# Optimization experiments

Measured on AMD Instinct MI355X. Metric: run time of the kernel, lower is better.

Reference implementation:

```python
import jax, jax.numpy as jnp
import numpy as np

B, N, D = 4096, 128, 256


def setup_inputs() -> dict:
    key = jax.random.key(0)
    ks = jax.random.split(key, 6)
    return {
        "label": jax.random.normal(ks[0], (B, N, D), dtype=jnp.float32),
        "adj_in": jax.random.uniform(ks[1], (N, N), dtype=jnp.float32),
        "adj_out": jax.random.uniform(ks[2], (N, N), dtype=jnp.float32),
        "edge_bias": jnp.zeros((N, D), dtype=jnp.float32),
        "gate_weight": jax.random.normal(ks[3], (D, 1), dtype=jnp.float32) * (6.0 / (D + 1)) ** 0.5,
        "bias_gate": jnp.zeros((N, 1), dtype=jnp.float32),
        "out_edge_bias": jnp.zeros((N, D), dtype=jnp.float32),
        "out_gate_weight": jax.random.normal(ks[4], (D, 1), dtype=jnp.float32) * (6.0 / (D + 1)) ** 0.5,
        "out_bias_gate": jnp.zeros((N, 1), dtype=jnp.float32),
        "loop_gate": jax.random.normal(ks[5], (D, 1), dtype=jnp.float32) * (6.0 / (D + 1)) ** 0.5,
    }


def reference(label, adj_in, adj_out, edge_bias, gate_weight, bias_gate,
              out_edge_bias, out_gate_weight, out_bias_gate, loop_gate):
    h = label  # [B, N, D]
    # origin_adj is a constant buffer in the original module (detached numpy)
    origin = jax.lax.stop_gradient(jnp.where(adj_in <= 0, adj_in, 1.0))

    # in-arc branch: masked dense adjacency matmul + bias + scalar gate
    h_in = jnp.einsum('mn,bnd->bmd', origin * adj_in, h)            # [B, N, D]
    in_gate = jnp.einsum('bnd,do->bno', h, gate_weight) + bias_gate  # [B, N, 1]
    msg_in = (h_in + edge_bias) * jax.nn.sigmoid(in_gate)

    # out-arc branch: transposed mask times out adjacency
    h_out = jnp.einsum('mn,bnd->bmd', origin.T * adj_out, h)
    out_gate = jnp.einsum('bnd,do->bno', h, out_gate_weight) + out_bias_gate
    msg_out = (h_out + out_edge_bias) * jax.nn.sigmoid(out_gate)

    # self-loop branch
    lp_gate = jnp.einsum('bnd,do->bno', h, loop_gate)
    msg_loop = h * jax.nn.sigmoid(lp_gate)

    # dropout p=0.0 -> identity
    return jax.nn.relu(msg_in + msg_out + msg_loop)
```

## Files before the change

kernel.cpp:

```cpp
#include <hip/hip_runtime.h>
#include <hip/hip_bf16.h>

#define NN 128
#define ND 256

typedef __attribute__((ext_vector_type(8))) short short8v;
typedef __attribute__((ext_vector_type(4))) short short4v;
typedef __attribute__((ext_vector_type(4))) float floatx4;

__device__ __forceinline__ unsigned short f2bf(float x){
  unsigned u = __float_as_uint(x);
  u += 0x7FFF + ((u >> 16) & 1);
  return (unsigned short)(u >> 16);
}
__device__ __forceinline__ float bf2f(unsigned short h){
  return __uint_as_float(((unsigned)h) << 16);
}

__global__ void prep_A(const float* __restrict__ adj_in, const float* __restrict__ adj_out,
                       const float* __restrict__ gw, const float* __restrict__ ogw,
                       const float* __restrict__ lw, unsigned short* __restrict__ Abf){
  int idx = blockIdx.x * 256 + threadIdx.x;
  if (idx < 32768){
    int m = idx >> 7, n = idx & 127;
    float v;
    if (m < NN){
      float a = adj_in[m * NN + n];
      v = (a <= 0.f) ? a * a : a;
    } else {
      int mm = m - NN;
      float t = adj_in[n * NN + mm];
      float o = (t <= 0.f) ? t : 1.f;
      v = o * adj_out[mm * NN + n];
    }
    Abf[idx] = f2bf(v);
  } else if (idx < 32768 + 4096){
    int t   = idx - 32768;
    int j   = t & 7, m16 = (t >> 3) & 15, g = (t >> 7) & 3, kc = t >> 9;
    int d   = kc * 32 + 8 * g + j;
    float v = (m16 == 0) ? gw[d] : (m16 == 1) ? ogw[d] : (m16 == 2) ? lw[d] : 0.f;
    Abf[idx] = f2bf(v);
  }
}

__global__ __launch_bounds__(512, 4) void gcn_main(
    const float* __restrict__ H, const unsigned short* __restrict__ Abf,
    const float* __restrict__ eb,  const float* __restrict__ bg,
    const float* __restrict__ oeb, const float* __restrict__ obg,
    float* __restrict__ Out)
{
  __shared__ __align__(16) unsigned short Ht[ND * NN];
  __shared__ float sigS[3 * NN];

  const int tid  = threadIdx.x;
  const int wave = tid >> 6;
  const int lane = tid & 63;
  const int g    = lane >> 4;
  const int m16  = lane & 15;
  const int b    = blockIdx.x;
  const float* Hb = H   + (size_t)b * NN * ND;
  float*       Ob = Out + (size_t)b * NN * ND;
  const unsigned short* WgT = Abf + 32768;

  const int G    = 4 * wave + g;
  const int n0   = 4 * G;
  const int arow = 16 * wave + m16;

  floatx4 gacc = {0.f, 0.f, 0.f, 0.f};
  #pragma unroll
  for (int s = 0; s < 4; ++s){
    #pragma unroll
    for (int t = 0; t < 2; ++t){
      const int k0 = 64 * s + 32 * t;
      const floatx4 f0 = *(const floatx4*)(Hb + (size_t)arow * ND + k0 + 8 * g);
      const floatx4 f1 = *(const floatx4*)(Hb + (size_t)arow * ND + k0 + 8 * g + 4);
      const short8v wv = *(const short8v*)&WgT[(((k0 >> 5) * 4 + g) * 16 + m16) * 8];
      short8v af;
      af[0] = (short)f2bf(f0[0]); af[1] = (short)f2bf(f0[1]);
      af[2] = (short)f2bf(f0[2]); af[3] = (short)f2bf(f0[3]);
      af[4] = (short)f2bf(f1[0]); af[5] = (short)f2bf(f1[1]);
      af[6] = (short)f2bf(f1[2]); af[7] = (short)f2bf(f1[3]);
      gacc = __builtin_amdgcn_mfma_f32_16x16x32_bf16(af, wv, gacc, 0, 0, 0);
    }
    const int d0 = 64 * s + 4 * m16;
    floatx4 rr[4];
    #pragma unroll
    for (int ro = 0; ro < 4; ++ro)
      rr[ro] = *(const floatx4*)(Hb + (size_t)(n0 + ro) * ND + d0);
    #pragma unroll
    for (int j = 0; j < 4; ++j){
      const int d = d0 + j;
      short4v pv;
      pv[0] = (short)f2bf(rr[0][j]);
      pv[1] = (short)f2bf(rr[1][j]);
      pv[2] = (short)f2bf(rr[2][j]);
      pv[3] = (short)f2bf(rr[3][j]);
      *(short4v*)&Ht[d * NN + (n0 ^ (((d >> 1) & 7) << 3))] = pv;
    }
  }
  if (m16 < 3){
    #pragma unroll
    for (int r = 0; r < 4; ++r){
      const int n = 16 * wave + 4 * g + r;
      float x = gacc[r];
      if (m16 == 0)      x += bg[n];
      else if (m16 == 1) x += obg[n];
      sigS[m16 * NN + n] = 1.f / (1.f + __expf(-x));
    }
  }
  __syncthreads();

  const float si = sigS[arow];
  const float so = sigS[NN + arow];
  const float sl = sigS[2 * NN + arow];

  const floatx4 zz = {0.f, 0.f, 0.f, 0.f};
  #pragma unroll
  for (int pass = 0; pass < 2; ++pass){
    const int dbase = 128 * pass;
    floatx4 acc1[8], acc2[8];
    #pragma unroll
    for (int i = 0; i < 8; ++i){ acc1[i] = zz; acc2[i] = zz; }

    #pragma unroll
    for (int k0 = 0; k0 < 128; k0 += 32){
      const int kk = k0 + 8 * g;
      const short8v av1 = *(const short8v*)&Abf[ arow        * 128 + kk];
      const short8v av2 = *(const short8v*)&Abf[(128 + arow) * 128 + kk];
      #pragma unroll
      for (int df = 0; df < 8; ++df){
        const int d = dbase + 16 * df + m16;
        const short8v hv = *(const short8v*)&Ht[d * NN + (kk ^ (((d >> 1) & 7) << 3))];
        acc1[df] = __builtin_amdgcn_mfma_f32_16x16x32_bf16(hv, av1, acc1[df], 0, 0, 0);
        acc2[df] = __builtin_amdgcn_mfma_f32_16x16x32_bf16(hv, av2, acc2[df], 0, 0, 0);
      }
    }

    #pragma unroll
    for (int df = 0; df < 8; ++df){
      const int dcol = dbase + 16 * df + 4 * g;
      const floatx4 ebv  = *(const floatx4*)(eb  + arow * ND + dcol);
      const floatx4 oebv = *(const floatx4*)(oeb + arow * ND + dcol);
      float hl[4];
      #pragma unroll
      for (int r = 0; r < 4; ++r){
        const int d = dcol + r;
        hl[r] = bf2f(Ht[d * NN + (arow ^ (((d >> 1) & 7) << 3))]);
      }
      floatx4 o;
      #pragma unroll
      for (int r = 0; r < 4; ++r){
        const float v = (acc1[df][r] + ebv[r]) * si
                      + (acc2[df][r] + oebv[r]) * so
                      + hl[r] * sl;
        o[r] = fmaxf(v, 0.f);
      }
      __builtin_nontemporal_store(o, (floatx4*)(Ob + (size_t)arow * ND + dcol));
    }
  }
}

extern "C" void kernel_launch(void* const* d_in, const int* in_sizes, int n_in,
                              void* d_out, int out_size, void* d_ws, size_t ws_size,
                              hipStream_t stream){
  const float* H    = (const float*)d_in[0];
  const float* ain  = (const float*)d_in[1];
  const float* aout = (const float*)d_in[2];
  const float* eb   = (const float*)d_in[3];
  const float* gwp  = (const float*)d_in[4];
  const float* bgp  = (const float*)d_in[5];
  const float* oebp = (const float*)d_in[6];
  const float* ogwp = (const float*)d_in[7];
  const float* obgp = (const float*)d_in[8];
  const float* lwp  = (const float*)d_in[9];
  unsigned short* Abf = (unsigned short*)d_ws;

  prep_A<<<144, 256, 0, stream>>>(ain, aout, gwp, ogwp, lwp, Abf);
  gcn_main<<<4096, 512, 0, stream>>>(H, Abf, eb, bgp, oebp, obgp, (float*)d_out);
}
```

Measured before the change: 373.8 us.

## Retune staging, swizzle, block order, and epilogue of the fused GCN kernel

Measured after the change: 409.2 us. +9.5%, slower.

```diff
diff --git a/kernel.cpp b/kernel.cpp
--- a/kernel.cpp
+++ b/kernel.cpp
@@ -4,9 +4,12 @@
 #define NN 128
 #define ND 256
 
+#define SWZ(d) ((((d) ^ ((d) >> 2)) & 15) << 3)
+
 typedef __attribute__((ext_vector_type(8))) short short8v;
-typedef __attribute__((ext_vector_type(4))) short short4v;
 typedef __attribute__((ext_vector_type(4))) float floatx4;
+typedef __attribute__((ext_vector_type(2))) unsigned int uint2v;
+typedef __attribute__((ext_vector_type(4))) unsigned int uint4v;
 
 __device__ __forceinline__ unsigned short f2bf(float x){
   unsigned u = __float_as_uint(x);
@@ -15,6 +18,13 @@
 }
 __device__ __forceinline__ float bf2f(unsigned short h){
   return __uint_as_float(((unsigned)h) << 16);
+}
+__device__ __forceinline__ unsigned pk2(float a, float b){
+  float2 t; t.x = a; t.y = b;
+  __hip_bfloat162 hh = __float22bfloat162_rn(t);
+  unsigned r;
+  __builtin_memcpy(&r, &hh, 4);
+  return r;
 }
 
 __global__ void prep_A(const float* __restrict__ adj_in, const float* __restrict__ adj_out,
@@ -57,45 +67,47 @@
   const int lane = tid & 63;
   const int g    = lane >> 4;
   const int m16  = lane & 15;
-  const int b    = blockIdx.x;
+  const int b    = (blockIdx.x & 7) * 512 + (blockIdx.x >> 3);
   const float* Hb = H   + (size_t)b * NN * ND;
   float*       Ob = Out + (size_t)b * NN * ND;
   const unsigned short* WgT = Abf + 32768;
 
-  const int G    = 4 * wave + g;
-  const int n0   = 4 * G;
+  const int n0   = 4 * (4 * wave + g);
   const int arow = 16 * wave + m16;
 
   floatx4 gacc = {0.f, 0.f, 0.f, 0.f};
   #pragma unroll
-  for (int s = 0; s < 4; ++s){
+  for (int s = 0; s < 2; ++s){
+    const int ds0 = 128 * s;
+    floatx4 rr[2][4];
     #pragma unroll
-    for (int t = 0; t < 2; ++t){
-      const int k0 = 64 * s + 32 * t;
+    for (int dq = 0; dq < 2; ++dq)
+      #pragma unroll
+      for (int ro = 0; ro < 4; ++ro)
+        rr[dq][ro] = *(const floatx4*)(Hb + (size_t)(n0 + ro) * ND + ds0 + 64 * dq + 4 * m16);
+    #pragma unroll
+    for (int t = 0; t < 4; ++t){
+      const int k0 = ds0 + 32 * t;
+      const short8v wv = *(const short8v*)&WgT[(((k0 >> 5) * 4 + g) * 16 + m16) * 8];
       const floatx4 f0 = *(const floatx4*)(Hb + (size_t)arow * ND + k0 + 8 * g);
       const floatx4 f1 = *(const floatx4*)(Hb + (size_t)arow * ND + k0 + 8 * g + 4);
-      const short8v wv = *(const short8v*)&WgT[(((k0 >> 5) * 4 + g) * 16 + m16) * 8];
+      uint4v au;
+      au[0] = pk2(f0[0], f0[1]); au[1] = pk2(f0[2], f0[3]);
+      au[2] = pk2(f1[0], f1[1]); au[3] = pk2(f1[2], f1[3]);
       short8v af;
-      af[0] = (short)f2bf(f0[0]); af[1] = (short)f2bf(f0[1]);
-      af[2] = (short)f2bf(f0[2]); af[3] = (short)f2bf(f0[3]);
-      af[4] = (short)f2bf(f1[0]); af[5] = (short)f2bf(f1[1]);
-      af[6] = (short)f2bf(f1[2]); af[7] = (short)f2bf(f1[3]);
+      __builtin_memcpy(&af, &au, 16);
       gacc = __builtin_amdgcn_mfma_f32_16x16x32_bf16(af, wv, gacc, 0, 0, 0);
     }
-    const int d0 = 64 * s + 4 * m16;
-    floatx4 rr[4];
     #pragma unroll
-    for (int ro = 0; ro < 4; ++ro)
-      rr[ro] = *(const floatx4*)(Hb + (size_t)(n0 + ro) * ND + d0);
-    #pragma unroll
-    for (int j = 0; j < 4; ++j){
-      const int d = d0 + j;
-      short4v pv;
-      pv[0] = (short)f2bf(rr[0][j]);
-      pv[1] = (short)f2bf(rr[1][j]);
-      pv[2] = (short)f2bf(rr[2][j]);
-      pv[3] = (short)f2bf(rr[3][j]);
-      *(short4v*)&Ht[d * NN + (n0 ^ (((d >> 1) & 7) << 3))] = pv;
+    for (int dq = 0; dq < 2; ++dq){
+      #pragma unroll
+      for (int j = 0; j < 4; ++j){
+        const int d = ds0 + 64 * dq + 4 * m16 + j;
+        uint2v pv;
+        pv[0] = pk2(rr[dq][0][j], rr[dq][1][j]);
+        pv[1] = pk2(rr[dq][2][j], rr[dq][3][j]);
+        *(uint2v*)&Ht[d * NN + (n0 ^ SWZ(d))] = pv;
+      }
     }
   }
   if (m16 < 3){
@@ -114,48 +126,52 @@
   const float so = sigS[NN + arow];
   const float sl = sigS[2 * NN + arow];
 
-  const floatx4 zz = {0.f, 0.f, 0.f, 0.f};
   #pragma unroll
-  for (int pass = 0; pass < 2; ++pass){
-    const int dbase = 128 * pass;
-    floatx4 acc1[8], acc2[8];
+  for (int p = 0; p < 4; ++p){
+    floatx4 ebv[4], oebv[4];
     #pragma unroll
-    for (int i = 0; i < 8; ++i){ acc1[i] = zz; acc2[i] = zz; }
+    for (int df2 = 0; df2 < 4; ++df2){
+      const int dcol = 16 * (4 * p + df2) + 4 * g;
+      ebv[df2]  = *(const floatx4*)(eb  + arow * ND + dcol);
+      oebv[df2] = *(const floatx4*)(oeb + arow * ND + dcol);
+    }
 
+    floatx4 acc1[4], acc2[4];
+    #pragma unroll
+    for (int i = 0; i < 4; ++i){
+      acc1[i] = (floatx4){0.f,0.f,0.f,0.f};
+      acc2[i] = (floatx4){0.f,0.f,0.f,0.f};
+    }
+    __builtin_amdgcn_s_setprio(1);
     #pragma unroll
     for (int k0 = 0; k0 < 128; k0 += 32){
       const int kk = k0 + 8 * g;
       const short8v av1 = *(const short8v*)&Abf[ arow        * 128 + kk];
       const short8v av2 = *(const short8v*)&Abf[(128 + arow) * 128 + kk];
       #pragma unroll
-      for (int df = 0; df < 8; ++df){
-        const int d = dbase + 16 * df + m16;
-        const short8v hv = *(const short8v*)&Ht[d * NN + (kk ^ (((d >> 1) & 7) << 3))];
-        acc1[df] = __builtin_amdgcn_mfma_f32_16x16x32_bf16(hv, av1, acc1[df], 0, 0, 0);
-        acc2[df] = __builtin_amdgcn_mfma_f32_16x16x32_bf16(hv, av2, acc2[df], 0, 0, 0);
+      for (int df2 = 0; df2 < 4; ++df2){
+        const int d = 16 * (4 * p + df2) + m16;
+        const short8v hv = *(const short8v*)&Ht[d * NN + (kk ^ SWZ(d))];
+        acc1[df2] = __builtin_amdgcn_mfma_f32_16x16x32_bf16(hv, av1, acc1[df2], 0, 0, 0);
+        acc2[df2] = __builtin_amdgcn_mfma_f32_16x16x32_bf16(hv, av2, acc2[df2], 0, 0, 0);
       }
     }
+    __builtin_amdgcn_s_setprio(0);
 
     #pragma unroll
-    for (int df = 0; df < 8; ++df){
-      const int dcol = dbase + 16 * df + 4 * g;
-      const floatx4 ebv  = *(const floatx4*)(eb  + arow * ND + dcol);
-      const floatx4 oebv = *(const floatx4*)(oeb + arow * ND + dcol);
-      float hl[4];
+    for (int df2 = 0; df2 < 4; ++df2){
+      const int dcol = 16 * (4 * p + df2) + 4 * g;
+      floatx4 o;
       #pragma unroll
       for (int r = 0; r < 4; ++r){
         const int d = dcol + r;
-        hl[r] = bf2f(Ht[d * NN + (arow ^ (((d >> 1) & 7) << 3))]);
-      }
-      floatx4 o;
-      #pragma unroll
-      for (int r = 0; r < 4; ++r){
-        const float v = (acc1[df][r] + ebv[r]) * si
-                      + (acc2[df][r] + oebv[r]) * so
-                      + hl[r] * sl;
+        const float hl = bf2f(Ht[d * NN + (arow ^ SWZ(d))]);
+        const float v = (acc1[df2][r] + ebv[df2][r]) * si
+                      + (acc2[df2][r] + oebv[df2][r]) * so
+                      + hl * sl;
         o[r] = fmaxf(v, 0.f);
       }
-      __builtin_nontemporal_store(o, (floatx4*)(Ob + (size_t)arow * ND + dcol));
+      *(floatx4*)(Ob + (size_t)arow * ND + dcol) = o;
     }
   }
 }
```
